# Performance work log

Hardware: AMD Instinct MI355X
Metric: run time of the kernel (lower is better)

The kernel has to match this reference:

```python
import jax, jax.numpy as jnp
import numpy as np

B, C_IN, H, W = 8, 256, 64, 64
REL, OUT, SHARE, K = 32, 256, 8, 3
G = OUT // SHARE          # 32 groups
MID = REL * (K * K + 1)   # 320, conv_w input channels
WOUT = K * K * OUT // SHARE  # 288, conv_w output channels
EPS = 1e-5


def _conv1x1(x, w, b=None):
    # x: [B,C,H,W], w: [O,C]
    y = jnp.einsum('bchw,oc->bohw', x, w)
    if b is not None:
        y = y + b[None, :, None, None]
    return y


def _bn(x, g, b, m, v):
    scale = g / jnp.sqrt(v + EPS)
    return x * scale[None, :, None, None] + (b - m * scale)[None, :, None, None]


def _unfold3(xp):
    # xp: [B,C,H+2,W+2] (already padded) -> [B,C,9,H,W], torch Unfold channel-major order
    h, w = xp.shape[2] - 2, xp.shape[3] - 2
    return jnp.stack([xp[:, :, i:i + h, j:j + w] for i in range(K) for j in range(K)], axis=2)


def setup_inputs() -> dict:
    key = jax.random.key(0)
    ks = jax.random.split(key, 24)
    n = lambda k, sh, s=0.05: jax.random.normal(k, sh, jnp.float32) * s
    u = lambda k, sh: jax.random.uniform(k, sh, jnp.float32, 0.5, 1.5)
    return {
        'x': jax.random.normal(ks[0], (B, C_IN, H, W), jnp.float32),
        'w1': n(ks[1], (REL, C_IN)), 'b1': n(ks[2], (REL,)),
        'w2': n(ks[3], (REL, C_IN)), 'b2': n(ks[4], (REL,)),
        'w3': n(ks[5], (OUT, C_IN)), 'b3': n(ks[6], (OUT,)),
        'bn1_g': u(ks[7], (MID,)), 'bn1_b': n(ks[8], (MID,)),
        'bn1_m': n(ks[9], (MID,)), 'bn1_v': u(ks[10], (MID,)),
        'cw1': n(ks[11], (G, MID)),
        'bn2_g': u(ks[12], (G,)), 'bn2_b': n(ks[13], (G,)),
        'bn2_m': n(ks[14], (G,)), 'bn2_v': u(ks[15], (G,)),
        'cw2': n(ks[16], (WOUT, G)), 'cb2': n(ks[17], (WOUT,)),
    }


def reference(x, w1, b1, w2, b2, w3, b3,
              bn1_g, bn1_b, bn1_m, bn1_v, cw1,
              bn2_g, bn2_b, bn2_m, bn2_v, cw2, cb2):
    x1 = _conv1x1(x, w1, b1)            # [B,REL,H,W]
    x2 = _conv1x1(x, w2, b2)            # [B,REL,H,W]
    x3 = _conv1x1(x, w3, b3)            # [B,OUT,H,W]

    # reflect-pad + unfold x2 -> [B, REL*9, H, W]
    x2p = jnp.pad(x2, ((0, 0), (0, 0), (1, 1), (1, 1)), mode='reflect')
    x2u = _unfold3(x2p).reshape(B, REL * K * K, H, W)

    # weight generator: BN-ReLU-1x1-BN-ReLU-1x1
    h = jnp.concatenate([x1, x2u], axis=1)          # [B, 320, H, W]
    h = jax.nn.relu(_bn(h, bn1_g, bn1_b, bn1_m, bn1_v))
    h = _conv1x1(h, cw1)                             # [B, 32, H, W]
    h = jax.nn.relu(_bn(h, bn2_g, bn2_b, bn2_m, bn2_v))
    w = _conv1x1(h, cw2, cb2)                        # [B, 288, H, W]
    w = w.reshape(B, G, K * K, H, W)                 # per-pixel kernels per group

    # local convolution: zero-pad unfold of x3, grouped gather-multiply-reduce
    x3p = jnp.pad(x3, ((0, 0), (0, 0), (1, 1), (1, 1)))
    x3u = _unfold3(x3p).reshape(B, G, SHARE, K * K, H, W)
    out = jnp.einsum('bgskhw,bgkhw->bgshw', x3u, w).reshape(B, OUT, H, W)
    return out
```

## Files before the change

### kernel.cpp

```cpp
#include <hip/hip_runtime.h>

typedef unsigned short u16;
typedef unsigned int   u32;

#define B_    8
#define CIN   256
#define G_    32
#define MID_  320
#define WOUT_ 288
#define EPS_  1e-5f

typedef __attribute__((ext_vector_type(8))) short bf16x8;
typedef __attribute__((ext_vector_type(4))) float f32x4;

__device__ __forceinline__ float b2f(u16 v)  { return __uint_as_float(((u32)v) << 16); }
__device__ __forceinline__ u16   f2bf(float f) {
    u32 u = __float_as_uint(f);
    u += 0x7fffu + ((u >> 16) & 1u);
    return (u16)(u >> 16);
}
__device__ __forceinline__ float ldv(const void* p, int i, int isf32) {
    return isf32 ? ((const float*)p)[i] : b2f(((const u16*)p)[i]);
}
__device__ __forceinline__ int detect_f32(const void* bn1v) {
    const u32* p = (const u32*)bn1v;
    int allb = 1;
    #pragma unroll
    for (int i = 0; i < 16; ++i) {
        u32 lo = p[i] & 0xffffu;
        if (lo < 0x3F00u || lo > 0x3FC0u) allb = 0;
    }
    return allb ? 0 : 1;
}

#define OFF_Y     0u
#define OFF_BF    (22u<<20)
#define OFF_WLOC  (39u<<20)
#define PAR_OFF   (58u<<20)
#define BIAS_OFF  (PAR_OFF + 0u)
#define S1_OFF    (PAR_OFF + 1280u)
#define T1_OFF    (PAR_OFF + 2560u)
#define S2_OFF    (PAR_OFF + 3840u)
#define T2_OFF    (PAR_OFF + 3968u)
#define CB2_OFF   (PAR_OFF + 4096u)
#define CW1F_OFF  (PAR_OFF + 5248u)
#define CW2F_OFF  (PAR_OFF + 25728u)
#define WF_OFF    (PAR_OFF + 44160u)

__global__ __launch_bounds__(256) void prep_k(
    const void* __restrict__ x,
    const void* __restrict__ w1, const void* __restrict__ b1,
    const void* __restrict__ w2, const void* __restrict__ b2,
    const void* __restrict__ w3, const void* __restrict__ b3,
    const void* __restrict__ bn1g, const void* __restrict__ bn1b,
    const void* __restrict__ bn1m, const void* __restrict__ bn1v,
    const void* __restrict__ cw1,
    const void* __restrict__ bn2g, const void* __restrict__ bn2b,
    const void* __restrict__ bn2m, const void* __restrict__ bn2v,
    const void* __restrict__ cw2, const void* __restrict__ cb2,
    u16* __restrict__ Bfrag, u16* __restrict__ Wfrag,
    float* __restrict__ biasAll, float* __restrict__ s1, float* __restrict__ t1,
    u16* __restrict__ cw1f, float* __restrict__ s2, float* __restrict__ t2,
    u16* __restrict__ cw2f, float* __restrict__ cb2f)
{
    __shared__ int sflag;
    const int t = threadIdx.x;
    if (t == 0) sflag = detect_f32(bn1v);
    __syncthreads();
    const int isf32 = sflag;
    const int bid = blockIdx.x;

    if (bid < 2048) {
        __shared__ u16 tile[64 * 70];
        const int pt = bid & 63, ct = (bid >> 6) & 3, b = bid >> 8;
        const int c0 = ct * 64, hw0 = pt * 64;
        if (isf32) {
            const float* xf = (const float*)x;
            for (int p = 0; p < 8; ++p) {
                int idx = t + 256 * p;
                int i = idx >> 5, j2 = idx & 31;
                float2 v = *(const float2*)&xf[((b * 256 + c0 + i) * 4096) + hw0 + 2 * j2];
                *(u32*)&tile[i * 70 + 2 * j2] = (u32)f2bf(v.x) | ((u32)f2bf(v.y) << 16);
            }
        } else {
            const u32* xh = (const u32*)x;
            for (int p = 0; p < 8; ++p) {
                int idx = t + 256 * p;
                int i = idx >> 5, j2 = idx & 31;
                *(u32*)&tile[i * 70 + 2 * j2] = xh[(((b * 256 + c0 + i) * 4096) + hw0) / 2 + j2];
            }
        }
        __syncthreads();
        #pragma unroll
        for (int p = 0; p < 2; ++p) {
            int idx = t + 256 * p;
            int q = idx >> 6, lane = idx & 63;
            int t16l = q >> 1, ksl = q & 1;
            int l16 = lane & 15, quad = lane >> 4;
            u16 tmp[8];
            #pragma unroll
            for (int j = 0; j < 8; ++j)
                tmp[j] = tile[(ksl * 32 + quad * 8 + j) * 70 + t16l * 16 + l16];
            uint4 pk = make_uint4((u32)tmp[0] | ((u32)tmp[1] << 16),
                                  (u32)tmp[2] | ((u32)tmp[3] << 16),
                                  (u32)tmp[4] | ((u32)tmp[5] << 16),
                                  (u32)tmp[6] | ((u32)tmp[7] << 16));
            size_t flat = ((size_t)((b * 256 + pt * 4 + t16l) * 8 + ct * 2 + ksl) * 64 + lane) * 8;
            *(uint4*)&Bfrag[flat] = pk;
        }
        return;
    }

    {
        const int wb = bid - 2048;
        for (int f = wb * 1280 + t; f < (wb + 1) * 1280 * 0 + wb * 1280 + 1280; f += 256) {
            int j = f & 7, lane = (f >> 3) & 63, ks = (f >> 9) & 7, mtile = f >> 12;
            int oc = mtile * 16 + (lane & 15);
            int c = ks * 32 + (lane >> 4) * 8 + j;
            float v;
            if (oc < 32)       v = ldv(w1, oc * CIN + c, isf32);
            else if (oc < 64)  v = ldv(w2, (oc - 32) * CIN + c, isf32);
            else               v = ldv(w3, (oc - 64) * CIN + c, isf32);
            Wfrag[f] = f2bf(v);
        }
    }
    if (bid != 2048) return;

    for (int oc = t; oc < MID_; oc += 256) {
        float bb;
        if (oc < 32)       bb = ldv(b1, oc, isf32);
        else if (oc < 64)  bb = ldv(b2, oc - 32, isf32);
        else               bb = ldv(b3, oc - 64, isf32);
        biasAll[oc] = bb;
        float g = ldv(bn1g, oc, isf32), v = ldv(bn1v, oc, isf32);
        float m = ldv(bn1m, oc, isf32), be = ldv(bn1b, oc, isf32);
        float s = g * rsqrtf(v + EPS_);
        s1[oc] = s;
        t1[oc] = be - m * s;
    }
    for (int g = t; g < G_; g += 256) {
        float gg = ldv(bn2g, g, isf32), v = ldv(bn2v, g, isf32);
        float m = ldv(bn2m, g, isf32), be = ldv(bn2b, g, isf32);
        float s = gg * rsqrtf(v + EPS_);
        s2[g] = s;
        t2[g] = be - m * s;
    }
    for (int o = t; o < WOUT_; o += 256)
        cb2f[o] = ldv(cb2, o, isf32);
    for (int f = t; f < 10240; f += 256) {
        int j = f & 7, lane = (f >> 3) & 63, half = (f >> 9) & 1, ks2 = f >> 10;
        int g = half * 16 + (lane & 15);
        int k = ks2 * 32 + (lane >> 4) * 8 + j;
        cw1f[f] = f2bf(ldv(cw1, g * MID_ + k, isf32));
    }
    for (int f = t; f < 9216; f += 256) {
        int j = f & 7, lane = (f >> 3) & 63, nn = (f >> 9) & 1, nc = f >> 10;
        int o = nc * 32 + nn * 16 + (lane & 15);
        int gk = (lane >> 4) * 8 + j;
        cw2f[f] = f2bf(ldv(cw2, o * G_ + gk, isf32));
    }
}

__global__ __launch_bounds__(256) void conv_k(
    const u16* __restrict__ Wfrag, const u16* __restrict__ Bfrag,
    const float* __restrict__ biasAll, u16* __restrict__ y)
{
    const int pt = blockIdx.x, mt5 = blockIdx.y, b = blockIdx.z;
    const int oc0 = mt5 * 64, pxb = pt * 256;
    const int t = threadIdx.x;
    const int lane = t & 63, wv = t >> 6;
    const int l16 = lane & 15, quad = lane >> 4;

    f32x4 acc[4][4];
    #pragma unroll
    for (int i = 0; i < 4; ++i)
        #pragma unroll
        for (int j = 0; j < 4; ++j) acc[i][j] = (f32x4){0.f, 0.f, 0.f, 0.f};

    const u16* abase = Wfrag + (size_t)(mt5 * 4) * 8 * 512;
    const u16* bbase = Bfrag + (size_t)((b * 256 + pt * 16 + wv * 4)) * 8 * 512;

    #pragma unroll
    for (int ks = 0; ks < 8; ++ks) {
        bf16x8 af[4], bfr[4];
        #pragma unroll
        for (int mtl = 0; mtl < 4; ++mtl)
            af[mtl] = *(const bf16x8*)&abase[((mtl * 8 + ks) * 64 + lane) * 8];
        #pragma unroll
        for (int nt = 0; nt < 4; ++nt)
            bfr[nt] = *(const bf16x8*)&bbase[((nt * 8 + ks) * 64 + lane) * 8];
        #pragma unroll
        for (int mtl = 0; mtl < 4; ++mtl)
            #pragma unroll
            for (int nt = 0; nt < 4; ++nt)
                acc[mtl][nt] = __builtin_amdgcn_mfma_f32_16x16x32_bf16(af[mtl], bfr[nt], acc[mtl][nt], 0, 0, 0);
    }
    float bias_r[4][4];
    #pragma unroll
    for (int mtl = 0; mtl < 4; ++mtl)
        #pragma unroll
        for (int r = 0; r < 4; ++r)
            bias_r[mtl][r] = biasAll[oc0 + mtl * 16 + quad * 4 + r];
    #pragma unroll
    for (int mtl = 0; mtl < 4; ++mtl) {
        int oc = oc0 + mtl * 16 + quad * 4;
        #pragma unroll
        for (int nt = 0; nt < 4; ++nt) {
            int px = pxb + wv * 64 + nt * 16 + l16;
            #pragma unroll
            for (int r = 0; r < 4; ++r)
                y[((b * 320) + oc + r) * 4096 + px] = f2bf(acc[mtl][nt][r] + bias_r[mtl][r]);
        }
    }
}

__global__ __launch_bounds__(256) void wgen_k(
    const u16* __restrict__ y, const u16* __restrict__ cw1f,
    const float* __restrict__ s1g, const float* __restrict__ t1g,
    const float* __restrict__ s2g, const float* __restrict__ t2g,
    const u16* __restrict__ cw2f, const float* __restrict__ cb2f,
    u16* __restrict__ wloc2)
{
    __shared__ u16 x2slab[32 * 3 * 64];
    __shared__ u16 chunk[64 * 72];
    __shared__ float s1s[320], t1s[320];
    __shared__ u32 lut[320];
    __shared__ u16 aATs[4 * 16 * 40];
    const int h = blockIdx.x, b = blockIdx.y;
    const int t = threadIdx.x;
    const int lane = t & 63, wv = t >> 6;
    const int l16 = lane & 15, quad = lane >> 4;
    const int hw0 = h * 64;

    {
        const u32* yw = (const u32*)y;
        for (int i = t; i < 3072; i += 256) {
            int r = i / 96, rem = i - r * 96;
            int i3 = rem >> 5, pw = rem & 31;
            int hr = h + i3 - 1; hr = hr < 0 ? 1 : (hr > 63 ? 62 : hr);
            u32 v = yw[(((b * 320) + 32 + r) * 4096 + hr * 64) / 2 + pw];
            *(u32*)&x2slab[(r * 3 + i3) * 64 + pw * 2] = v;
        }
    }
    for (int i = t; i < 320; i += 256) { s1s[i] = s1g[i]; t1s[i] = t1g[i]; }
    for (int k = t; k < 320; k += 256) {
        u32 v;
        if (k < 32) v = 0xFFFFFFFFu;
        else {
            int cc = k - 32;
            int r = cc / 9, tt = cc - 9 * r;
            int i3 = tt / 3, j3 = tt - 3 * i3;
            v = (((u32)((r * 3 + i3) * 64)) << 2) | (u32)j3;
        }
        lut[k] = v;
    }
    __syncthreads();

    const int kp = t >> 3;
    const int wb = t & 7;
    f32x4 acc0 = {0.f,0.f,0.f,0.f}, acc1 = {0.f,0.f,0.f,0.f};

    for (int ks5 = 0; ks5 < 5; ++ks5) {
        const int kbase = ks5 * 64;
        #pragma unroll
        for (int j = 0; j < 8; ++j) {
            const int w = wb + 8 * j;
            const int wm = (w == 0) ? 1 : w - 1;
            const int wp = (w == 63) ? 62 : w + 1;
            u16 vv[2];
            #pragma unroll
            for (int e = 0; e < 2; ++e) {
                const int k = kbase + 2 * kp + e;
                u32 lv = lut[k];
                float xval;
                if (lv == 0xFFFFFFFFu)
                    xval = b2f(y[((b * 320) + k) * 4096 + hw0 + w]);
                else {
                    int j3 = (int)(lv & 3u);
                    int base = (int)(lv >> 2);
                    int wj = (j3 == 0) ? wm : ((j3 == 1) ? w : wp);
                    xval = b2f(x2slab[base + wj]);
                }
                vv[e] = f2bf(fmaxf(s1s[k] * xval + t1s[k], 0.f));
            }
            *(u32*)&chunk[w * 72 + kp * 2] = (u32)vv[0] | ((u32)vv[1] << 16);
        }
        __syncthreads();
        #pragma unroll
        for (int ks = 0; ks < 2; ++ks) {
            const int ks2 = ks5 * 2 + ks;
            bf16x8 af = *(const bf16x8*)&chunk[(wv * 16 + l16) * 72 + ks * 32 + quad * 8];
            bf16x8 b0 = *(const bf16x8*)&cw1f[((ks2 * 2 + 0) * 64 + lane) * 8];
            bf16x8 b1 = *(const bf16x8*)&cw1f[((ks2 * 2 + 1) * 64 + lane) * 8];
            acc0 = __builtin_amdgcn_mfma_f32_16x16x32_bf16(af, b0, acc0, 0, 0, 0);
            acc1 = __builtin_amdgcn_mfma_f32_16x16x32_bf16(af, b1, acc1, 0, 0, 0);
        }
        __syncthreads();
    }

    u16* aw = &aATs[wv * 16 * 40];
    {
        float sg0 = s2g[l16],      tg0 = t2g[l16];
        float sg1 = s2g[16 + l16], tg1 = t2g[16 + l16];
        #pragma unroll
        for (int r = 0; r < 4; ++r) {
            aw[(quad * 4 + r) * 40 + l16]      = f2bf(fmaxf(sg0 * acc0[r] + tg0, 0.f));
            aw[(quad * 4 + r) * 40 + 16 + l16] = f2bf(fmaxf(sg1 * acc1[r] + tg1, 0.f));
        }
    }
    __syncthreads();
    bf16x8 aaf = *(const bf16x8*)&aw[l16 * 40 + quad * 8];

    const int pxs = wv * 16 + quad * 4;
    for (int nc = 0; nc < 9; ++nc) {
        f32x4 c0 = {0.f,0.f,0.f,0.f}, c1 = {0.f,0.f,0.f,0.f};
        bf16x8 b0 = *(const bf16x8*)&cw2f[((nc * 2 + 0) * 64 + lane) * 8];
        bf16x8 b1 = *(const bf16x8*)&cw2f[((nc * 2 + 1) * 64 + lane) * 8];
        c0 = __builtin_amdgcn_mfma_f32_16x16x32_bf16(aaf, b0, c0, 0, 0, 0);
        c1 = __builtin_amdgcn_mfma_f32_16x16x32_bf16(aaf, b1, c1, 0, 0, 0);
        float cb0 = cb2f[nc * 32 + l16];
        float cb1 = cb2f[nc * 32 + 16 + l16];
        #pragma unroll
        for (int r = 0; r < 4; ++r) {
            const u32 base = ((u32)((b * 4096) + hw0 + pxs + r)) * 288u + (u32)(nc * 32);
            wloc2[base + l16]      = f2bf(c0[r] + cb0);
            wloc2[base + 16 + l16] = f2bf(c1[r] + cb1);
        }
    }
}

__global__ __launch_bounds__(256) void lconv_k(
    const u16* __restrict__ y, const u16* __restrict__ wloc2,
    const void* __restrict__ bn1v, void* __restrict__ outv)
{
    __shared__ u16 x3s[8 * 34 * 64];
    __shared__ int sflag;
    const int hf = blockIdx.x, g = blockIdx.y, b = blockIdx.z;
    const int h0 = hf * 32;
    const int t = threadIdx.x;
    if (t == 0) sflag = detect_f32(bn1v);

    {
        const u32* yw = (const u32*)y;
        int s = t >> 5, l = t & 31;
        int ch = 64 + g * 8 + s;
        for (int q = 0; q < 34; ++q) {
            int hr = h0 + q - 1;
            u32 v = 0;
            if (hr >= 0 && hr < 64) v = yw[(((b * 320) + ch) * 4096 + hr * 64) / 2 + l];
            *(u32*)&x3s[(s * 34 + q) * 64 + l * 2] = v;
        }
    }
    __syncthreads();
    const int isf32 = sflag;

    for (int q = 0; q < 8; ++q) {
        int px = t + 256 * q;
        int hl = px >> 6, w = px & 63;
        float wv9[9];
        const u16* wp = &wloc2[((u32)((b * 4096) + h0 * 64 + px)) * 288u + (u32)(g * 9)];
        #pragma unroll
        for (int k = 0; k < 9; ++k) wv9[k] = b2f(wp[k]);
        #pragma unroll
        for (int s = 0; s < 8; ++s) {
            float acc = 0.f;
            #pragma unroll
            for (int i3 = 0; i3 < 3; ++i3) {
                const u16* rowp = &x3s[(s * 34 + hl + i3) * 64];
                float a0 = (w > 0)  ? b2f(rowp[w - 1]) : 0.f;
                float a1 = b2f(rowp[w]);
                float a2 = (w < 63) ? b2f(rowp[w + 1]) : 0.f;
                acc += wv9[i3 * 3 + 0] * a0 + wv9[i3 * 3 + 1] * a1 + wv9[i3 * 3 + 2] * a2;
            }
            int oidx = ((b * 256) + g * 8 + s) * 4096 + h0 * 64 + px;
            if (isf32) ((float*)outv)[oidx] = acc;
            else       ((u16*)outv)[oidx] = f2bf(acc);
        }
    }
}

extern "C" void kernel_launch(void* const* d_in, const int* in_sizes, int n_in,
                              void* d_out, int out_size, void* d_ws, size_t ws_size,
                              hipStream_t stream) {
    (void)in_sizes; (void)n_in; (void)out_size; (void)ws_size;
    char* ws = (char*)d_ws;
    u16*   yb     = (u16*)  (ws + OFF_Y);
    u16*   Bfrag  = (u16*)  (ws + OFF_BF);
    u16*   wloc2  = (u16*)  (ws + OFF_WLOC);
    float* biasAll= (float*)(ws + BIAS_OFF);
    float* s1     = (float*)(ws + S1_OFF);
    float* t1     = (float*)(ws + T1_OFF);
    float* s2     = (float*)(ws + S2_OFF);
    float* t2     = (float*)(ws + T2_OFF);
    float* cb2f   = (float*)(ws + CB2_OFF);
    u16*   cw1f   = (u16*)  (ws + CW1F_OFF);
    u16*   cw2f   = (u16*)  (ws + CW2F_OFF);
    u16*   Wfrag  = (u16*)  (ws + WF_OFF);

    hipLaunchKernelGGL(prep_k, dim3(2112), dim3(256), 0, stream,
                       d_in[0],
                       d_in[1], d_in[2], d_in[3], d_in[4], d_in[5], d_in[6],
                       d_in[7], d_in[8], d_in[9], d_in[10], d_in[11],
                       d_in[12], d_in[13], d_in[14], d_in[15], d_in[16], d_in[17],
                       Bfrag, Wfrag, biasAll, s1, t1, cw1f, s2, t2, cw2f, cb2f);
    hipLaunchKernelGGL(conv_k, dim3(16, 5, 8), dim3(256), 0, stream,
                       Wfrag, Bfrag, biasAll, yb);
    hipLaunchKernelGGL(wgen_k, dim3(64, 8), dim3(256), 0, stream,
                       yb, cw1f, s1, t1, s2, t2, cw2f, cb2f, wloc2);
    hipLaunchKernelGGL(lconv_k, dim3(2, 32, 8), dim3(256), 0, stream,
                       yb, wloc2, d_in[10], d_out);
}
```

Before: 197.0 us.

## Build MFMA A-fragments in registers and store per-pixel weights channel-major

Measured after the change: 198.2 us. Within noise of the previous version (+0.6%).

```diff
diff --git a/kernel.cpp b/kernel.cpp
--- a/kernel.cpp
+++ b/kernel.cpp
@@ -113,7 +113,7 @@
 
     {
         const int wb = bid - 2048;
-        for (int f = wb * 1280 + t; f < (wb + 1) * 1280 * 0 + wb * 1280 + 1280; f += 256) {
+        for (int f = wb * 1280 + t; f < wb * 1280 + 1280; f += 256) {
             int j = f & 7, lane = (f >> 3) & 63, ks = (f >> 9) & 7, mtile = f >> 12;
             int oc = mtile * 16 + (lane & 15);
             int c = ks * 32 + (lane >> 4) * 8 + j;
@@ -219,10 +219,9 @@
     const float* __restrict__ s1g, const float* __restrict__ t1g,
     const float* __restrict__ s2g, const float* __restrict__ t2g,
     const u16* __restrict__ cw2f, const float* __restrict__ cb2f,
-    u16* __restrict__ wloc2)
+    u16* __restrict__ wloc)
 {
-    __shared__ u16 x2slab[32 * 3 * 64];
-    __shared__ u16 chunk[64 * 72];
+    __shared__ u16 mslab[128 * 66];
     __shared__ float s1s[320], t1s[320];
     __shared__ u32 lut[320];
     __shared__ u16 aATs[4 * 16 * 40];
@@ -239,63 +238,60 @@
             int i3 = rem >> 5, pw = rem & 31;
             int hr = h + i3 - 1; hr = hr < 0 ? 1 : (hr > 63 ? 62 : hr);
             u32 v = yw[(((b * 320) + 32 + r) * 4096 + hr * 64) / 2 + pw];
-            *(u32*)&x2slab[(r * 3 + i3) * 64 + pw * 2] = v;
+            *(u32*)&mslab[(r * 3 + i3) * 66 + pw * 2] = v;
+        }
+        for (int i = t; i < 1024; i += 256) {
+            int c = i >> 5, pw = i & 31;
+            u32 v = yw[(((b * 320) + c) * 4096 + hw0) / 2 + pw];
+            *(u32*)&mslab[(96 + c) * 66 + pw * 2] = v;
         }
     }
     for (int i = t; i < 320; i += 256) { s1s[i] = s1g[i]; t1s[i] = t1g[i]; }
     for (int k = t; k < 320; k += 256) {
         u32 v;
-        if (k < 32) v = 0xFFFFFFFFu;
+        if (k < 32) v = (((u32)((96 + k) * 66)) << 2) | 1u;
         else {
             int cc = k - 32;
-            int r = cc / 9, tt = cc - 9 * r;
-            int i3 = tt / 3, j3 = tt - 3 * i3;
-            v = (((u32)((r * 3 + i3) * 64)) << 2) | (u32)j3;
+            int r = cc / 9, tt2 = cc - 9 * r;
+            int i3 = tt2 / 3, j3 = tt2 - 3 * i3;
+            v = (((u32)((r * 3 + i3) * 66)) << 2) | (u32)j3;
         }
         lut[k] = v;
     }
     __syncthreads();
 
-    const int kp = t >> 3;
-    const int wb = t & 7;
+    const int w = wv * 16 + l16;
+    const int wm = (w == 0) ? 1 : w - 1;
+    const int wp = (w == 63) ? 62 : w + 1;
+
     f32x4 acc0 = {0.f,0.f,0.f,0.f}, acc1 = {0.f,0.f,0.f,0.f};
 
     for (int ks5 = 0; ks5 < 5; ++ks5) {
-        const int kbase = ks5 * 64;
-        #pragma unroll
-        for (int j = 0; j < 8; ++j) {
-            const int w = wb + 8 * j;
-            const int wm = (w == 0) ? 1 : w - 1;
-            const int wp = (w == 63) ? 62 : w + 1;
-            u16 vv[2];
+        union { u32 u[4]; bf16x8 v; } af[2];
+        #pragma unroll
+        for (int half = 0; half < 2; ++half) {
             #pragma unroll
-            for (int e = 0; e < 2; ++e) {
-                const int k = kbase + 2 * kp + e;
+            for (int j = 0; j < 8; ++j) {
+                const int k = ks5 * 64 + half * 32 + quad * 8 + j;
                 u32 lv = lut[k];
-                float xval;
-                if (lv == 0xFFFFFFFFu)
-                    xval = b2f(y[((b * 320) + k) * 4096 + hw0 + w]);
-                else {
-                    int j3 = (int)(lv & 3u);
-                    int base = (int)(lv >> 2);
-                    int wj = (j3 == 0) ? wm : ((j3 == 1) ? w : wp);
-                    xval = b2f(x2slab[base + wj]);
-                }
-                vv[e] = f2bf(fmaxf(s1s[k] * xval + t1s[k], 0.f));
+                int j3 = (int)(lv & 3u);
+                int base = (int)(lv >> 2);
+                int wj = (j3 == 0) ? wm : ((j3 == 1) ? w : wp);
+                float xval = b2f(mslab[base + wj]);
+                u16 hv = f2bf(fmaxf(s1s[k] * xval + t1s[k], 0.f));
+                if (j & 1) af[half].u[j >> 1] |= ((u32)hv << 16);
+                else       af[half].u[j >> 1]  = (u32)hv;
             }
-            *(u32*)&chunk[w * 72 + kp * 2] = (u32)vv[0] | ((u32)vv[1] << 16);
-        }
-        __syncthreads();
-        #pragma unroll
-        for (int ks = 0; ks < 2; ++ks) {
-            const int ks2 = ks5 * 2 + ks;
-            bf16x8 af = *(const bf16x8*)&chunk[(wv * 16 + l16) * 72 + ks * 32 + quad * 8];
-            bf16x8 b0 = *(const bf16x8*)&cw1f[((ks2 * 2 + 0) * 64 + lane) * 8];
-            bf16x8 b1 = *(const bf16x8*)&cw1f[((ks2 * 2 + 1) * 64 + lane) * 8];
-            acc0 = __builtin_amdgcn_mfma_f32_16x16x32_bf16(af, b0, acc0, 0, 0, 0);
-            acc1 = __builtin_amdgcn_mfma_f32_16x16x32_bf16(af, b1, acc1, 0, 0, 0);
-        }
-        __syncthreads();
+        }
+        const int ks2 = ks5 * 2;
+        bf16x8 b00 = *(const bf16x8*)&cw1f[(((ks2 + 0) * 2 + 0) * 64 + lane) * 8];
+        bf16x8 b01 = *(const bf16x8*)&cw1f[(((ks2 + 0) * 2 + 1) * 64 + lane) * 8];
+        bf16x8 b10 = *(const bf16x8*)&cw1f[(((ks2 + 1) * 2 + 0) * 64 + lane) * 8];
+        bf16x8 b11 = *(const bf16x8*)&cw1f[(((ks2 + 1) * 2 + 1) * 64 + lane) * 8];
+        acc0 = __builtin_amdgcn_mfma_f32_16x16x32_bf16(af[0].v, b00, acc0, 0, 0, 0);
+        acc1 = __builtin_amdgcn_mfma_f32_16x16x32_bf16(af[0].v, b01, acc1, 0, 0, 0);
+        acc0 = __builtin_amdgcn_mfma_f32_16x16x32_bf16(af[1].v, b10, acc0, 0, 0, 0);
+        acc1 = __builtin_amdgcn_mfma_f32_16x16x32_bf16(af[1].v, b11, acc1, 0, 0, 0);
     }
 
     u16* aw = &aATs[wv * 16 * 40];
@@ -311,7 +307,7 @@
     __syncthreads();
     bf16x8 aaf = *(const bf16x8*)&aw[l16 * 40 + quad * 8];
 
-    const int pxs = wv * 16 + quad * 4;
+    const int px0 = hw0 + wv * 16 + quad * 4;
     for (int nc = 0; nc < 9; ++nc) {
         f32x4 c0 = {0.f,0.f,0.f,0.f}, c1 = {0.f,0.f,0.f,0.f};
         bf16x8 b0 = *(const bf16x8*)&cw2f[((nc * 2 + 0) * 64 + lane) * 8];
@@ -320,17 +316,19 @@
         c1 = __builtin_amdgcn_mfma_f32_16x16x32_bf16(aaf, b1, c1, 0, 0, 0);
         float cb0 = cb2f[nc * 32 + l16];
         float cb1 = cb2f[nc * 32 + 16 + l16];
-        #pragma unroll
-        for (int r = 0; r < 4; ++r) {
-            const u32 base = ((u32)((b * 4096) + hw0 + pxs + r)) * 288u + (u32)(nc * 32);
-            wloc2[base + l16]      = f2bf(c0[r] + cb0);
-            wloc2[base + 16 + l16] = f2bf(c1[r] + cb1);
-        }
+        u16 q0 = f2bf(c0[0] + cb0), q1 = f2bf(c0[1] + cb0);
+        u16 q2 = f2bf(c0[2] + cb0), q3 = f2bf(c0[3] + cb0);
+        uint2 pk0 = make_uint2((u32)q0 | ((u32)q1 << 16), (u32)q2 | ((u32)q3 << 16));
+        *(uint2*)&wloc[(((size_t)(b * 288 + nc * 32 + l16)) << 12) + px0] = pk0;
+        u16 r0 = f2bf(c1[0] + cb1), r1 = f2bf(c1[1] + cb1);
+        u16 r2 = f2bf(c1[2] + cb1), r3 = f2bf(c1[3] + cb1);
+        uint2 pk1 = make_uint2((u32)r0 | ((u32)r1 << 16), (u32)r2 | ((u32)r3 << 16));
+        *(uint2*)&wloc[(((size_t)(b * 288 + nc * 32 + 16 + l16)) << 12) + px0] = pk1;
     }
 }
 
 __global__ __launch_bounds__(256) void lconv_k(
-    const u16* __restrict__ y, const u16* __restrict__ wloc2,
+    const u16* __restrict__ y, const u16* __restrict__ wloc,
     const void* __restrict__ bn1v, void* __restrict__ outv)
 {
     __shared__ u16 x3s[8 * 34 * 64];
@@ -357,10 +355,11 @@
     for (int q = 0; q < 8; ++q) {
         int px = t + 256 * q;
         int hl = px >> 6, w = px & 63;
+        int pxg = h0 * 64 + px;
         float wv9[9];
-        const u16* wp = &wloc2[((u32)((b * 4096) + h0 * 64 + px)) * 288u + (u32)(g * 9)];
-        #pragma unroll
-        for (int k = 0; k < 9; ++k) wv9[k] = b2f(wp[k]);
+        #pragma unroll
+        for (int k = 0; k < 9; ++k)
+            wv9[k] = b2f(wloc[(((size_t)(b * 288 + g * 9 + k)) << 12) + pxg]);
         #pragma unroll
         for (int s = 0; s < 8; ++s) {
             float acc = 0.f;
@@ -372,7 +371,7 @@
                 float a2 = (w < 63) ? b2f(rowp[w + 1]) : 0.f;
                 acc += wv9[i3 * 3 + 0] * a0 + wv9[i3 * 3 + 1] * a1 + wv9[i3 * 3 + 2] * a2;
             }
-            int oidx = ((b * 256) + g * 8 + s) * 4096 + h0 * 64 + px;
+            int oidx = ((b * 256) + g * 8 + s) * 4096 + pxg;
             if (isf32) ((float*)outv)[oidx] = acc;
             else       ((u16*)outv)[oidx] = f2bf(acc);
         }
@@ -386,7 +385,7 @@
     char* ws = (char*)d_ws;
     u16*   yb     = (u16*)  (ws + OFF_Y);
     u16*   Bfrag  = (u16*)  (ws + OFF_BF);
-    u16*   wloc2  = (u16*)  (ws + OFF_WLOC);
+    u16*   wlocb  = (u16*)  (ws + OFF_WLOC);
     float* biasAll= (float*)(ws + BIAS_OFF);
     float* s1     = (float*)(ws + S1_OFF);
     float* t1     = (float*)(ws + T1_OFF);
@@ -406,7 +405,7 @@
     hipLaunchKernelGGL(conv_k, dim3(16, 5, 8), dim3(256), 0, stream,
                        Wfrag, Bfrag, biasAll, yb);
     hipLaunchKernelGGL(wgen_k, dim3(64, 8), dim3(256), 0, stream,
-                       yb, cw1f, s1, t1, s2, t2, cw2f, cb2f, wloc2);
+                       yb, cw1f, s1, t1, s2, t2, cw2f, cb2f, wlocb);
     hipLaunchKernelGGL(lconv_k, dim3(2, 32, 8), dim3(256), 0, stream,
-                       yb, wloc2, d_in[10], d_out);
-}
+                       yb, wlocb, d_in[10], d_out);
+}
```
